# Kernel tuning notes

Measured on AMD Instinct MI355X. Metric: run time of the kernel, lower is better.

## Reference

```python
import jax, jax.numpy as jnp
import numpy as np

N, D, H, L, T, R = 50000, 128, 8, 2, 4, 8
E = 800000
HD = D // H  # head_size = 16
SQRT_D = float(np.sqrt(HD))


def typed_linear(x, types, W):
    # x: (n, Din), types: (n,), W: (T, Din, Dout)  -- per-type dense projection
    out = jnp.zeros((x.shape[0], W.shape[-1]), x.dtype)
    for t in range(W.shape[0]):
        out = out + jnp.where((types == t)[:, None], x @ W[t], 0.0)
    return out


def rel_typed(x, etype, W):
    # x: (E, H, d), etype: (E,), W: (H, R, d, d) -- per-head, per-edge-type linear
    out = jnp.zeros_like(x)
    for r in range(W.shape[1]):
        out = out + jnp.where((etype == r)[:, None, None], jnp.einsum('ehd,hdo->eho', x, W[:, r]), 0.0)
    return out


def edge_softmax(a, dst, n):
    # softmax over incoming edges per destination node, per head. a: (E, H)
    amax = jax.ops.segment_max(a, dst, num_segments=n)
    amax = jnp.where(jnp.isfinite(amax), amax, 0.0)
    ex = jnp.exp(a - amax[dst])
    s = jax.ops.segment_sum(ex, dst, num_segments=n)
    return ex / (s[dst] + 1e-9)


def layer_norm(x, g, b, eps=1e-5):
    mu = x.mean(-1, keepdims=True)
    var = ((x - mu) ** 2).mean(-1, keepdims=True)
    return (x - mu) * jax.lax.rsqrt(var + eps) * g + b


def hgt_conv(x, ntype, etype, src, dst, Wk, Wq, Wv, Wa, ratt, rmsg, rpri, skip):
    n = x.shape[0]
    k = typed_linear(x, ntype, Wk).reshape(n, H, HD)
    q = typed_linear(x, ntype, Wq).reshape(n, H, HD)
    v = typed_linear(x, ntype, Wv).reshape(n, H, HD)
    kw = rel_typed(k[src], etype, ratt)               # (E, H, d)
    pri = rpri[:, etype].T                            # (E, H)
    a = (kw * q[dst]).sum(-1) * pri / SQRT_D          # (E, H)
    m = rel_typed(v[src], etype, rmsg)                # (E, H, d)
    att = edge_softmax(a, dst, n)                     # (E, H)
    h = jax.ops.segment_sum(m * att[..., None], dst, num_segments=n)
    h = h.reshape(n, D)
    h = typed_linear(h, ntype, Wa)                    # dropout off (eval)
    alpha = jax.nn.sigmoid(skip[ntype])[:, None]
    return h * alpha + x * (1.0 - alpha)


def setup_inputs() -> dict:
    key = jax.random.key(0)
    ks = jax.random.split(key, 12)
    g_lin = float(np.sqrt(2.0 / (D + D)))   # xavier-ish scale for D x D
    g_rel = float(np.sqrt(2.0 / (HD + HD)))
    g_emb = float(np.sqrt(2.0 / (N + D)))
    return {
        'embed': jax.random.normal(ks[0], (T, N, D), jnp.float32) * g_emb,
        'Wk': jax.random.normal(ks[1], (L, T, D, D), jnp.float32) * g_lin,
        'Wq': jax.random.normal(ks[2], (L, T, D, D), jnp.float32) * g_lin,
        'Wv': jax.random.normal(ks[3], (L, T, D, D), jnp.float32) * g_lin,
        'Wa': jax.random.normal(ks[4], (L, T, D, D), jnp.float32) * g_lin,
        'rel_att': jax.random.normal(ks[5], (L, H, R, HD, HD), jnp.float32) * g_rel,
        'rel_msg': jax.random.normal(ks[6], (L, H, R, HD, HD), jnp.float32) * g_rel,
        'rel_pri': jnp.ones((L, H, R), jnp.float32),
        'skip': jnp.ones((L, T), jnp.float32),
        'ln_g': jnp.ones((L, D), jnp.float32),
        'ln_b': jnp.zeros((L, D), jnp.float32),
        'src': jax.random.randint(ks[7], (E,), 0, N, jnp.int32),
        'dst': jax.random.randint(ks[8], (E,), 0, N, jnp.int32),
        'ntype': jax.random.randint(ks[9], (N,), 0, T, jnp.int32),
        'etype': jax.random.randint(ks[10], (E,), 0, R, jnp.int32),
    }


def reference(embed, Wk, Wq, Wv, Wa, rel_att, rel_msg, rel_pri, skip, ln_g, ln_b, src, dst, ntype, etype):
    # masked per-type embedding init: node gets row <rank-within-its-type> of its type table
    onehot = jax.nn.one_hot(ntype, T, dtype=jnp.int32)
    rank = jnp.take_along_axis(jnp.cumsum(onehot, axis=0), ntype[:, None], axis=1)[:, 0] - 1
    h = embed[ntype, rank]                            # (N, D)
    for l in range(L):
        h_prev = h
        hc = hgt_conv(h, ntype, etype, src, dst,
                      Wk[l], Wq[l], Wv[l], Wa[l],
                      rel_att[l], rel_msg[l], rel_pri[l], skip[l])
        h = layer_norm(hc, ln_g[l], ln_b[l]) + h_prev
    return h
```

## Files before the change

### kernel.cpp

```cpp
#include <hip/hip_runtime.h>
#include <math.h>

#define N_NODES 50000
#define DIM     128
#define NHEAD   8
#define HDIM    16
#define NLAYER  2
#define NTYPE   4
#define NREL    8
#define NEDGE   800000
#define RB      256
#define GN      8
#define MT      32
#define NK      (N_NODES * NREL)

typedef __attribute__((ext_vector_type(8))) short bf16x8;
typedef __attribute__((ext_vector_type(4))) float f32x4;

__device__ __forceinline__ float blo(unsigned w) { return __uint_as_float(w << 16); }
__device__ __forceinline__ float bhi(unsigned w) { return __uint_as_float(w & 0xFFFF0000u); }
__device__ __forceinline__ unsigned short f2bf(float f) {
    unsigned b = __float_as_uint(f);
    b += 0x7FFFu + ((b >> 16) & 1u);
    return (unsigned short)(b >> 16);
}
__device__ __forceinline__ bf16x8 pack8(float4 x0, float4 x1) {
    bf16x8 r;
    r[0] = (short)f2bf(x0.x); r[1] = (short)f2bf(x0.y);
    r[2] = (short)f2bf(x0.z); r[3] = (short)f2bf(x0.w);
    r[4] = (short)f2bf(x1.x); r[5] = (short)f2bf(x1.y);
    r[6] = (short)f2bf(x1.z); r[7] = (short)f2bf(x1.w);
    return r;
}


__global__ void k_hist(const int* __restrict__ ntype, int* __restrict__ hist, int n) {
    __shared__ int cnt[NTYPE];
    if (threadIdx.x < NTYPE) cnt[threadIdx.x] = 0;
    __syncthreads();
    int i = blockIdx.x * RB + threadIdx.x;
    if (i < n) atomicAdd(&cnt[ntype[i]], 1);
    __syncthreads();
    if (threadIdx.x < NTYPE) hist[blockIdx.x * NTYPE + threadIdx.x] = cnt[threadIdx.x];
}

__global__ void k_prefix(const int* __restrict__ hist, int* __restrict__ off, int nb) {
    int t = threadIdx.x;
    if (t >= NTYPE) return;
    int acc = 0;
    for (int b = 0; b < nb; b++) { off[b * NTYPE + t] = acc; acc += hist[b * NTYPE + t]; }
}

__global__ void k_rank(const int* __restrict__ ntype, const int* __restrict__ off,
                       int* __restrict__ rank, int n) {
    __shared__ int ty[RB];
    int i = blockIdx.x * RB + threadIdx.x;
    int t = (i < n) ? ntype[i] : -1;
    ty[threadIdx.x] = t;
    __syncthreads();
    if (i < n) {
        int c = 0;
        for (int j = 0; j < (int)threadIdx.x; j++) c += (ty[j] == t);
        rank[i] = off[blockIdx.x * NTYPE + t] + c;
    }
}

__global__ void k_embed(const float* __restrict__ embed, const int* __restrict__ ntype,
                        const int* __restrict__ rank, float* __restrict__ h) {
    int i = blockIdx.x;
    int t = ntype[i], r = rank[i];
    h[(size_t)i * DIM + threadIdx.x] = embed[((size_t)t * N_NODES + r) * DIM + threadIdx.x];
}

__global__ void k_typeoff(const int* __restrict__ hist, const int* __restrict__ boff,
                          int nb, int* __restrict__ typeoff) {
    if (threadIdx.x == 0 && blockIdx.x == 0) {
        int acc = 0;
        for (int t = 0; t < NTYPE; t++) {
            typeoff[t] = acc;
            acc += boff[(nb - 1) * NTYPE + t] + hist[(nb - 1) * NTYPE + t];
        }
    }
}

__global__ void k_perm(const int* __restrict__ ntype, const int* __restrict__ rank,
                       const int* __restrict__ typeoff, int* __restrict__ perm,
                       int* __restrict__ iperm, int n) {
    int i = blockIdx.x * 256 + threadIdx.x;
    if (i < n) {
        int p = typeoff[ntype[i]] + rank[i];
        perm[p] = i;
        iperm[i] = p;
    }
}


__global__ void k_deg2(const int* __restrict__ dst, const int* __restrict__ etype,
                       int* __restrict__ deg) {
    int e = blockIdx.x * 256 + threadIdx.x;
    if (e < NEDGE) atomicAdd(&deg[dst[e] * NREL + etype[e]], 1);
}

__global__ void k_scan1(const int* __restrict__ deg, int* __restrict__ rs,
                        int* __restrict__ bsum, int n) {
    __shared__ int sh[256];
    int i = blockIdx.x * 256 + threadIdx.x;
    int v = (i < n) ? deg[i] : 0;
    sh[threadIdx.x] = v;
    __syncthreads();
    for (int off = 1; off < 256; off <<= 1) {
        int x = (threadIdx.x >= off) ? sh[threadIdx.x - off] : 0;
        __syncthreads();
        sh[threadIdx.x] += x;
        __syncthreads();
    }
    if (i < n) rs[i] = sh[threadIdx.x] - v;
    if (threadIdx.x == 255) bsum[blockIdx.x] = sh[255];
}

__global__ void k_scan2b(int* __restrict__ bsum, int nb) {
    __shared__ int sh[256];
    __shared__ int carry;
    if (threadIdx.x == 0) carry = 0;
    __syncthreads();
    for (int base = 0; base < nb; base += 256) {
        int i = base + threadIdx.x;
        int v = (i < nb) ? bsum[i] : 0;
        sh[threadIdx.x] = v;
        __syncthreads();
        for (int off = 1; off < 256; off <<= 1) {
            int x = (threadIdx.x >= off) ? sh[threadIdx.x - off] : 0;
            __syncthreads();
            sh[threadIdx.x] += x;
            __syncthreads();
        }
        if (i < nb) bsum[i] = sh[threadIdx.x] - v + carry;
        __syncthreads();
        if (threadIdx.x == 0) carry += sh[255];
        __syncthreads();
    }
}

__global__ void k_scan3(int* __restrict__ rs, const int* __restrict__ bsum, int n) {
    int i = blockIdx.x * 256 + threadIdx.x;
    if (i < n) rs[i] += bsum[blockIdx.x];
    if (i == 0) rs[n] = NEDGE;
}

__global__ void k_scatter2(const int* __restrict__ src, const int* __restrict__ dst,
                           const int* __restrict__ etype, const int* __restrict__ iperm,
                           const int* __restrict__ rs,
                           int* __restrict__ cur, int* __restrict__ epk) {
    int e = blockIdx.x * 256 + threadIdx.x;
    if (e < NEDGE) {
        int et = etype[e];
        int key = dst[e] * NREL + et;
        int p = atomicAdd(&cur[key], 1);
        epk[rs[key] + p] = iperm[src[e]] | (et << 24);
    }
}


__global__ void k_rattB(const float* __restrict__ ratt, unsigned short* __restrict__ rattB) {
    int i = blockIdx.x * 256 + threadIdx.x;
    rattB[i] = f2bf(ratt[i]);
}

__global__ void k_rmsgT(const float* __restrict__ rmsg, float* __restrict__ rmsgT) {
    int b = blockIdx.x;
    int d = threadIdx.x >> 4, o = threadIdx.x & 15;
    rmsgT[b * 256 + o * 16 + d] = rmsg[b * 256 + d * 16 + o];
}

__global__ void k_packW_all(const float* __restrict__ Wk, const float* __restrict__ Wq,
                            const float* __restrict__ Wv, unsigned short* __restrict__ wpk) {
    int bid = blockIdx.x;
    int t = bid & 3;
    int m = (bid >> 2) % 3;
    int l = bid / 12;
    const float* W = (m == 0 ? Wk : (m == 1 ? Wq : Wv)) + ((size_t)l * NTYPE + t) * 16384;
    unsigned short* ob = wpk + (size_t)bid * 16384;
    for (int idx = threadIdx.x; idx < 16384; idx += 256) {
        int ct = idx >> 11, kc = (idx >> 9) & 3, ln = (idx >> 3) & 63, j = idx & 7;
        int k = kc * 32 + ((ln >> 4) << 3) + j;
        int c = ct * 16 + (ln & 15);
        ob[idx] = f2bf(W[k * 128 + c]);
    }
}


__global__ __launch_bounds__(256) void k_qkv_mfma(
        const float* __restrict__ h, const int* __restrict__ perm, const int* __restrict__ ntype,
        const float* __restrict__ Wk, const float* __restrict__ Wq, const float* __restrict__ Wv,
        const unsigned short* __restrict__ WkB, const unsigned short* __restrict__ WqB,
        const unsigned short* __restrict__ WvB, const float* __restrict__ rmsgT,
        unsigned short* __restrict__ kb, float* __restrict__ qout,
        unsigned short* __restrict__ vt, int n) {
    int tid = threadIdx.x;
    int base = blockIdx.x * MT;
    __shared__ int nodes_s[MT];
    __shared__ int types_s[MT];
    __shared__ float vs[MT][132];

    if (tid < MT) {
        int idx = base + tid;
        int nd = (idx < n) ? perm[idx] : -1;
        nodes_s[tid] = nd;
        types_s[tid] = (nd >= 0) ? ntype[nd] : -1;
    }
    __syncthreads();
    bool same = (nodes_s[MT - 1] >= 0) && (types_s[0] == types_s[MT - 1]);
    int l = tid & 63, w = tid >> 6;

    if (same) {
        int t = types_s[0];
        const unsigned short* wbk = WkB + (size_t)t * 16384;
        const unsigned short* wbq = WqB + (size_t)t * 16384;
        const unsigned short* wbv = WvB + (size_t)t * 16384;
        f32x4 acc[3][2][2];
        #pragma unroll
        for (int m = 0; m < 3; m++)
            #pragma unroll
            for (int a = 0; a < 2; a++)
                #pragma unroll
                for (int b = 0; b < 2; b++) {
                    acc[m][a][b][0] = 0.f; acc[m][a][b][1] = 0.f;
                    acc[m][a][b][2] = 0.f; acc[m][a][b][3] = 0.f;
                }
        #pragma unroll 1
        for (int kc = 0; kc < 4; kc++) {
            int koff = kc * 32 + ((l >> 4) << 3);
            int r0 = l & 15;
            const float4* p0 = (const float4*)(h + (size_t)nodes_s[r0] * DIM + koff);
            bf16x8 a0 = pack8(p0[0], p0[1]);
            const float4* p1 = (const float4*)(h + (size_t)nodes_s[16 + r0] * DIM + koff);
            bf16x8 a1 = pack8(p1[0], p1[1]);
            #pragma unroll
            for (int cti = 0; cti < 2; cti++) {
                int boff = ((w * 2 + cti) * 4 + kc) * 512 + l * 8;
                bf16x8 bk = *(const bf16x8*)(wbk + boff);
                acc[0][0][cti] = __builtin_amdgcn_mfma_f32_16x16x32_bf16(a0, bk, acc[0][0][cti], 0, 0, 0);
                acc[0][1][cti] = __builtin_amdgcn_mfma_f32_16x16x32_bf16(a1, bk, acc[0][1][cti], 0, 0, 0);
                bf16x8 bq = *(const bf16x8*)(wbq + boff);
                acc[1][0][cti] = __builtin_amdgcn_mfma_f32_16x16x32_bf16(a0, bq, acc[1][0][cti], 0, 0, 0);
                acc[1][1][cti] = __builtin_amdgcn_mfma_f32_16x16x32_bf16(a1, bq, acc[1][1][cti], 0, 0, 0);
                bf16x8 bv = *(const bf16x8*)(wbv + boff);
                acc[2][0][cti] = __builtin_amdgcn_mfma_f32_16x16x32_bf16(a0, bv, acc[2][0][cti], 0, 0, 0);
                acc[2][1][cti] = __builtin_amdgcn_mfma_f32_16x16x32_bf16(a1, bv, acc[2][1][cti], 0, 0, 0);
            }
        }
        #pragma unroll
        for (int mt = 0; mt < 2; mt++)
            #pragma unroll
            for (int cti = 0; cti < 2; cti++) {
                int col = w * 32 + cti * 16 + (l & 15);
                #pragma unroll
                for (int r = 0; r < 4; r++) {
                    int row = mt * 16 + ((l >> 4) << 2) + r;
                    size_t p = (size_t)(base + row) * DIM + col;
                    kb[p] = f2bf(acc[0][mt][cti][r]);
                    qout[p] = acc[1][mt][cti][r];
                    vs[row][col] = acc[2][mt][cti][r];
                }
            }
    } else {
        int o = tid & 127, half = tid >> 7;
        for (int nn = half; nn < MT; nn += 2) {
            int nd = nodes_s[nn];
            if (nd < 0) { vs[nn][o] = 0.f; continue; }
            int t = types_s[nn];
            const float* wk = Wk + (size_t)t * 16384;
            const float* wq = Wq + (size_t)t * 16384;
            const float* wv = Wv + (size_t)t * 16384;
            float ak = 0.f, aq = 0.f, av = 0.f;
            for (int d = 0; d < DIM; d++) {
                float xv = h[(size_t)nd * DIM + d];
                ak = fmaf(xv, wk[d * DIM + o], ak);
                aq = fmaf(xv, wq[d * DIM + o], aq);
                av = fmaf(xv, wv[d * DIM + o], av);
            }
            size_t p = (size_t)(base + nn) * DIM + o;
            kb[p] = f2bf(ak); qout[p] = aq;
            vs[nn][o] = av;
        }
    }
    __syncthreads();
    {
        int o = tid & 127, half = tid >> 7;
        int hh = o >> 4, oo = o & 15;
        #pragma unroll 1
        for (int et = 0; et < NREL; et++) {
            const float4* w4 = (const float4*)(rmsgT + ((size_t)(hh * NREL + et) * HDIM + oo) * HDIM);
            float4 w0 = w4[0], w1 = w4[1], w2 = w4[2], w3 = w4[3];
            for (int i = 0; i < 16; i++) {
                int nn = half * 16 + i;
                if (base + nn >= n) continue;
                const float4* v4 = (const float4*)&vs[nn][hh * HDIM];
                float4 v0 = v4[0], v1 = v4[1], v2 = v4[2], v3 = v4[3];
                float a2 = v0.x*w0.x + v0.y*w0.y + v0.z*w0.z + v0.w*w0.w
                         + v1.x*w1.x + v1.y*w1.y + v1.z*w1.z + v1.w*w1.w
                         + v2.x*w2.x + v2.y*w2.y + v2.z*w2.z + v2.w*w2.w
                         + v3.x*w3.x + v3.y*w3.y + v3.z*w3.z + v3.w*w3.w;
                vt[((size_t)(base + nn) * NREL + et) * DIM + o] = f2bf(a2);
            }
        }
    }
}


__global__ __launch_bounds__(128) void k_fused11(
        const unsigned short* __restrict__ kb, const float* __restrict__ qbuf,
        const unsigned short* __restrict__ vt,
        const int* __restrict__ perm,
        const int* __restrict__ rs2, const int* __restrict__ epk,
        const unsigned short* __restrict__ rattB, const float* __restrict__ rpri,
        float* __restrict__ agg) {
    int b = blockIdx.x;
    int node = perm[b];
    int tid = threadIdx.x;
    int hh = tid >> 4, oo = tid & 15;
    int wv = tid >> 6;
    int hl = hh & 3;

    __shared__ float q_s[DIM];
    __shared__ float u_s[NREL][NHEAD * HDIM + 4];
    __shared__ float a_sw[2][4][HDIM + 1];
    __shared__ int   es_sw[2][HDIM];

    int e0 = rs2[node * NREL];
    int e1 = rs2[node * NREL + NREL];
    if (e0 == e1) { agg[(size_t)b * DIM + tid] = 0.f; return; }

    q_s[tid] = qbuf[(size_t)b * DIM + tid];
    {
        const float4* q4 = (const float4*)&q_s[hh * HDIM];
        float4 q0 = q4[0], q1 = q4[1], q2 = q4[2], q3 = q4[3];
        #pragma unroll
        for (int et = 0; et < NREL; et++) {
            const uint4* wB = (const uint4*)(rattB + ((size_t)(hh * NREL + et) * HDIM + oo) * HDIM);
            uint4 wa = wB[0], wb = wB[1];
            float s = blo(wa.x)*q0.x + bhi(wa.x)*q0.y + blo(wa.y)*q0.z + bhi(wa.y)*q0.w
                    + blo(wa.z)*q1.x + bhi(wa.z)*q1.y + blo(wa.w)*q1.z + bhi(wa.w)*q1.w
                    + blo(wb.x)*q2.x + bhi(wb.x)*q2.y + blo(wb.y)*q2.z + bhi(wb.y)*q2.w
                    + blo(wb.z)*q3.x + bhi(wb.z)*q3.y + blo(wb.w)*q3.z + bhi(wb.w)*q3.w;
            u_s[et][tid] = s * rpri[hh * NREL + et] * 0.25f;
        }
    }

    float m_h = -1e30f, s_h = 0.f, out = 0.f;

    for (int w0e = e0; w0e < e1; w0e += HDIM) {
        int cnt = min(HDIM, e1 - w0e);
        float a = -1e30f;
        int pk = 0;
        if (oo < cnt) {
            pk = epk[w0e + oo];
            int sv = pk & 0x00FFFFFF;
            int et = ((unsigned)pk) >> 24;
            const uint4* kr = (const uint4*)(kb + (size_t)sv * DIM + hh * HDIM);
            uint4 ka = kr[0], kc = kr[1];
            const float4* u4 = (const float4*)&u_s[et][hh * HDIM];
            float4 u0 = u4[0], u1 = u4[1], u2 = u4[2], u3 = u4[3];
            a = blo(ka.x)*u0.x + bhi(ka.x)*u0.y + blo(ka.y)*u0.z + bhi(ka.y)*u0.w
              + blo(ka.z)*u1.x + bhi(ka.z)*u1.y + blo(ka.w)*u1.z + bhi(ka.w)*u1.w
              + blo(kc.x)*u2.x + bhi(kc.x)*u2.y + blo(kc.y)*u2.z + bhi(kc.y)*u2.w
              + blo(kc.z)*u3.x + bhi(kc.z)*u3.y + blo(kc.w)*u3.z + bhi(kc.w)*u3.w;
        }
        if (hl == 0) es_sw[wv][oo] = pk;
        float cmax = a;
        cmax = fmaxf(cmax, __shfl_xor(cmax, 1));
        cmax = fmaxf(cmax, __shfl_xor(cmax, 2));
        cmax = fmaxf(cmax, __shfl_xor(cmax, 4));
        cmax = fmaxf(cmax, __shfl_xor(cmax, 8));
        float m_t = (cmax > m_h + 12.f) ? cmax : m_h;
        float r = __expf(m_h - m_t);
        s_h *= r; out *= r; m_h = m_t;
        float p = (oo < cnt) ? __expf(a - m_h) : 0.f;
        float ps = p;
        ps += __shfl_xor(ps, 1);
        ps += __shfl_xor(ps, 2);
        ps += __shfl_xor(ps, 4);
        ps += __shfl_xor(ps, 8);
        s_h += ps;
        a_sw[wv][hl][oo] = p;
        for (int c = 0; c < cnt; c++) {
            float pc = a_sw[wv][hl][c];
            int pkc = es_sw[wv][c];
            int sv = pkc & 0x00FFFFFF;
            int et = ((unsigned)pkc) >> 24;
            unsigned short uv = vt[((size_t)sv * NREL + et) * DIM + tid];
            out = fmaf(pc, __uint_as_float((unsigned)uv << 16), out);
        }
    }

    agg[(size_t)b * DIM + tid] = out / (s_h + 1e-9f);
}


__global__ __launch_bounds__(128) void k_out_g(
        const float* __restrict__ agg, float* __restrict__ h,
        const int* __restrict__ perm, const int* __restrict__ ntype,
        const float* __restrict__ Wa, const float* __restrict__ skip,
        const float* __restrict__ ln_g, const float* __restrict__ ln_b, int n) {
    int o = threadIdx.x;
    int base = blockIdx.x * GN;
    __shared__ float xs[GN][DIM];
    __shared__ float hcs[GN][DIM + 1];
    __shared__ int nodes[GN];
    __shared__ int types[GN];
    __shared__ float mu_s[GN], rs_s[GN];
    if (o < GN) {
        int idx = base + o;
        int nd = (idx < n) ? perm[idx] : -1;
        nodes[o] = nd;
        types[o] = (nd >= 0) ? ntype[nd] : -1;
    }
    __syncthreads();
    #pragma unroll
    for (int nn = 0; nn < GN; nn++)
        if (nodes[nn] >= 0) xs[nn][o] = agg[(size_t)(base + nn) * DIM + o];
    __syncthreads();
    bool same = (nodes[GN - 1] >= 0) && (types[0] == types[GN - 1]);
    if (same) {
        int t = types[0];
        const float* w = Wa + (size_t)t * DIM * DIM;
        float acc[GN];
        #pragma unroll
        for (int nn = 0; nn < GN; nn++) acc[nn] = 0.f;
        for (int d = 0; d < DIM; d++) {
            float wv = w[d * DIM + o];
            #pragma unroll
            for (int nn = 0; nn < GN; nn++) acc[nn] = fmaf(xs[nn][d], wv, acc[nn]);
        }
        float alpha = 1.f / (1.f + __expf(-skip[t]));
        #pragma unroll
        for (int nn = 0; nn < GN; nn++) {
            float hp = h[(size_t)nodes[nn] * DIM + o];
            hcs[nn][o] = acc[nn] * alpha + hp * (1.f - alpha);
        }
    } else {
        #pragma unroll 1
        for (int nn = 0; nn < GN; nn++) {
            if (nodes[nn] < 0) continue;
            int t = types[nn];
            const float* w = Wa + (size_t)t * DIM * DIM;
            float a0 = 0.f;
            for (int d = 0; d < DIM; d++) a0 = fmaf(xs[nn][d], w[d * DIM + o], a0);
            float alpha = 1.f / (1.f + __expf(-skip[t]));
            float hp = h[(size_t)nodes[nn] * DIM + o];
            hcs[nn][o] = a0 * alpha + hp * (1.f - alpha);
        }
    }
    __syncthreads();
    {
        int g = o >> 4, j = o & 15;
        if (nodes[g] >= 0) {
            float s = 0.f;
            for (int d = j; d < DIM; d += 16) s += hcs[g][d];
            #pragma unroll
            for (int m = 1; m < 16; m <<= 1) s += __shfl_xor(s, m);
            float mu = s * (1.f / DIM);
            float v = 0.f;
            for (int d = j; d < DIM; d += 16) { float dv = hcs[g][d] - mu; v = fmaf(dv, dv, v); }
            #pragma unroll
            for (int m = 1; m < 16; m <<= 1) v += __shfl_xor(v, m);
            if (j == 0) { mu_s[g] = mu; rs_s[g] = rsqrtf(v * (1.f / DIM) + 1e-5f); }
        }
    }
    __syncthreads();
    float g_o = ln_g[o], b_o = ln_b[o];
    #pragma unroll
    for (int nn = 0; nn < GN; nn++) {
        if (nodes[nn] >= 0) {
            float hp = h[(size_t)nodes[nn] * DIM + o];
            h[(size_t)nodes[nn] * DIM + o] = (hcs[nn][o] - mu_s[nn]) * rs_s[nn] * g_o + b_o + hp;
        }
    }
}


extern "C" void kernel_launch(void* const* d_in, const int* in_sizes, int n_in,
                              void* d_out, int out_size, void* d_ws, size_t ws_size,
                              hipStream_t stream) {
    const float* embed = (const float*)d_in[0];
    const float* Wk    = (const float*)d_in[1];
    const float* Wq    = (const float*)d_in[2];
    const float* Wv    = (const float*)d_in[3];
    const float* Wa    = (const float*)d_in[4];
    const float* ratt  = (const float*)d_in[5];
    const float* rmsg  = (const float*)d_in[6];
    const float* rpri  = (const float*)d_in[7];
    const float* skip  = (const float*)d_in[8];
    const float* ln_g  = (const float*)d_in[9];
    const float* ln_b  = (const float*)d_in[10];
    const int*   src   = (const int*)d_in[11];
    const int*   dst   = (const int*)d_in[12];
    const int*   ntype = (const int*)d_in[13];
    const int*   etype = (const int*)d_in[14];

    float* h = (float*)d_out;

    const size_t ND = (size_t)N_NODES * DIM;
    const int nb = (N_NODES + RB - 1) / RB;
    unsigned short* kb = (unsigned short*)d_ws;
    float* qbuf = (float*)(kb + ND);
    int* rs2  = (int*)(qbuf + ND);
    int* deg2 = rs2 + (NK + 1);
    int* cur2 = deg2 + NK;
    int* epk  = cur2 + NK;
    int* bsum = epk + NEDGE;
    int* rank = bsum + 2048;
    int* hist = rank + N_NODES;
    int* boff = hist + nb * NTYPE;
    int* typeoff = boff + nb * NTYPE;
    int* perm = typeoff + NTYPE;
    int* iperm = perm + N_NODES;
    float* rmsgT = (float*)(iperm + N_NODES);
    unsigned short* rattB = (unsigned short*)(rmsgT + (size_t)NLAYER * NHEAD * NREL * 256);
    unsigned short* vt = rattB + (size_t)NLAYER * NHEAD * NREL * 256;
    unsigned short* wpk = vt + (size_t)N_NODES * NREL * DIM;
    float* agg = qbuf;

    const int EB = (NEDGE + 255) / 256;
    const int nb2 = (NK + 255) / 256;

    k_hist<<<nb, RB, 0, stream>>>(ntype, hist, N_NODES);
    k_prefix<<<1, 64, 0, stream>>>(hist, boff, nb);
    k_rank<<<nb, RB, 0, stream>>>(ntype, boff, rank, N_NODES);
    k_embed<<<N_NODES, DIM, 0, stream>>>(embed, ntype, rank, h);
    k_typeoff<<<1, 64, 0, stream>>>(hist, boff, nb, typeoff);
    k_perm<<<nb, 256, 0, stream>>>(ntype, rank, typeoff, perm, iperm, N_NODES);

    hipMemsetAsync(deg2, 0, (size_t)NK * sizeof(int), stream);
    hipMemsetAsync(cur2, 0, (size_t)NK * sizeof(int), stream);
    k_deg2<<<EB, 256, 0, stream>>>(dst, etype, deg2);
    k_scan1<<<nb2, 256, 0, stream>>>(deg2, rs2, bsum, NK);
    k_scan2b<<<1, 256, 0, stream>>>(bsum, nb2);
    k_scan3<<<nb2, 256, 0, stream>>>(rs2, bsum, NK);
    k_scatter2<<<EB, 256, 0, stream>>>(src, dst, etype, iperm, rs2, cur2, epk);

    k_rattB<<<NLAYER * NHEAD * NREL, 256, 0, stream>>>(ratt, rattB);
    k_rmsgT<<<NLAYER * NHEAD * NREL, 256, 0, stream>>>(rmsg, rmsgT);
    k_packW_all<<<NLAYER * 3 * NTYPE, 256, 0, stream>>>(Wk, Wq, Wv, wpk);

    const int NGB = N_NODES / GN;
    const int NMB = (N_NODES + MT - 1) / MT;

    for (int l = 0; l < NLAYER; l++) {
        const float* Wk_l = Wk + (size_t)l * NTYPE * DIM * DIM;
        const float* Wq_l = Wq + (size_t)l * NTYPE * DIM * DIM;
        const float* Wv_l = Wv + (size_t)l * NTYPE * DIM * DIM;
        const float* Wa_l = Wa + (size_t)l * NTYPE * DIM * DIM;
        const unsigned short* wkB_l = wpk + ((size_t)l * 3 + 0) * NTYPE * 16384;
        const unsigned short* wqB_l = wpk + ((size_t)l * 3 + 1) * NTYPE * 16384;
        const unsigned short* wvB_l = wpk + ((size_t)l * 3 + 2) * NTYPE * 16384;
        const unsigned short* rattB_l = rattB + (size_t)l * NHEAD * NREL * 256;
        const float* rmsgT_l = rmsgT + (size_t)l * NHEAD * NREL * 256;
        const float* rpri_l = rpri + (size_t)l * NHEAD * NREL;
        const float* skip_l = skip + (size_t)l * NTYPE;
        const float* g_l = ln_g + (size_t)l * DIM;
        const float* b_l = ln_b + (size_t)l * DIM;

        k_qkv_mfma<<<NMB, 256, 0, stream>>>(h, perm, ntype, Wk_l, Wq_l, Wv_l,
                                            wkB_l, wqB_l, wvB_l, rmsgT_l,
                                            kb, qbuf, vt, N_NODES);
        k_fused11<<<N_NODES, 128, 0, stream>>>(kb, qbuf, vt, perm, rs2, epk,
                                               rattB_l, rpri_l, agg);
        k_out_g<<<NGB, 128, 0, stream>>>(agg, h, perm, ntype, Wa_l, skip_l, g_l, b_l, N_NODES);
    }
}
```

Measured before the change: 755.6 us.

## Precompute per-relation key and message tables per node with MFMA

Instead of applying the per-head, per-relation att and msg matrices on every edge in the aggregation kernel, the QKV kernel now computes transformed K and V for all 8 relation types per node using MFMA, with priority and 1/sqrt(d) folded into the att weights. A new edge kernel simply gathers the precomputed bf16 rows by (src, etype). This trades per-edge matmul work for a much larger node-side table write and gather bandwidth. The path is only enabled when the workspace is large enough, otherwise the old path is used.

```diff
diff --git a/kernel.cpp b/kernel.cpp
--- a/kernel.cpp
+++ b/kernel.cpp
@@ -13,6 +13,7 @@
 #define GN      8
 #define MT      32
 #define NK      (N_NODES * NREL)
+#define LHR     (NLAYER * NHEAD * NREL)
 
 typedef __attribute__((ext_vector_type(8))) short bf16x8;
 typedef __attribute__((ext_vector_type(4))) float f32x4;
@@ -30,6 +31,12 @@
     r[2] = (short)f2bf(x0.z); r[3] = (short)f2bf(x0.w);
     r[4] = (short)f2bf(x1.x); r[5] = (short)f2bf(x1.y);
     r[6] = (short)f2bf(x1.z); r[7] = (short)f2bf(x1.w);
+    return r;
+}
+__device__ __forceinline__ bf16x8 zero8() {
+    bf16x8 r;
+    #pragma unroll
+    for (int j = 0; j < 8; j++) r[j] = 0;
     return r;
 }
 
@@ -170,6 +177,31 @@
     int b = blockIdx.x;
     int d = threadIdx.x >> 4, o = threadIdx.x & 15;
     rmsgT[b * 256 + o * 16 + d] = rmsg[b * 256 + d * 16 + o];
+}
+
+__global__ void k_rmsgBP(const float* __restrict__ rmsg, unsigned short* __restrict__ out) {
+    int b = blockIdx.x;
+    int i = threadIdx.x;
+    int ln = i >> 3, e = i & 7;
+    int half = ln >> 4;
+    unsigned short v = 0;
+    if (half < 2) v = f2bf(rmsg[(size_t)b * 256 + (half * 8 + e) * 16 + (ln & 15)]);
+    out[(size_t)b * 512 + i] = v;
+}
+
+__global__ void k_rattBP(const float* __restrict__ ratt, const float* __restrict__ rpri,
+                         unsigned short* __restrict__ out) {
+    int b = blockIdx.x;
+    int i = threadIdx.x;
+    int ln = i >> 3, e = i & 7;
+    int half = ln >> 4;
+    int et = b % NREL;
+    int hh = (b / NREL) % NHEAD;
+    int l = b / (NREL * NHEAD);
+    float scale = rpri[(l * NHEAD + hh) * NREL + et] * 0.25f;
+    unsigned short v = 0;
+    if (half < 2) v = f2bf(ratt[(size_t)b * 256 + (half * 8 + e) * 16 + (ln & 15)] * scale);
+    out[(size_t)b * 512 + i] = v;
 }
 
 __global__ void k_packW_all(const float* __restrict__ Wk, const float* __restrict__ Wq,
@@ -189,18 +221,21 @@
 }
 
 
+template<int FULL>
 __global__ __launch_bounds__(256) void k_qkv_mfma(
         const float* __restrict__ h, const int* __restrict__ perm, const int* __restrict__ ntype,
         const float* __restrict__ Wk, const float* __restrict__ Wq, const float* __restrict__ Wv,
         const unsigned short* __restrict__ WkB, const unsigned short* __restrict__ WqB,
         const unsigned short* __restrict__ WvB, const float* __restrict__ rmsgT,
+        const unsigned short* __restrict__ rattBP, const unsigned short* __restrict__ rmsgBP,
         unsigned short* __restrict__ kb, float* __restrict__ qout,
-        unsigned short* __restrict__ vt, int n) {
+        unsigned short* __restrict__ vt, unsigned short* __restrict__ tab, int n) {
     int tid = threadIdx.x;
     int base = blockIdx.x * MT;
     __shared__ int nodes_s[MT];
     __shared__ int types_s[MT];
     __shared__ float vs[MT][132];
+    __shared__ float ks[MT][132];
 
     if (tid < MT) {
         int idx = base + tid;
@@ -258,16 +293,17 @@
                 for (int r = 0; r < 4; r++) {
                     int row = mt * 16 + ((l >> 4) << 2) + r;
                     size_t p = (size_t)(base + row) * DIM + col;
-                    kb[p] = f2bf(acc[0][mt][cti][r]);
                     qout[p] = acc[1][mt][cti][r];
                     vs[row][col] = acc[2][mt][cti][r];
+                    if constexpr (FULL) ks[row][col] = acc[0][mt][cti][r];
+                    else                kb[p] = f2bf(acc[0][mt][cti][r]);
                 }
             }
     } else {
         int o = tid & 127, half = tid >> 7;
         for (int nn = half; nn < MT; nn += 2) {
             int nd = nodes_s[nn];
-            if (nd < 0) { vs[nn][o] = 0.f; continue; }
+            if (nd < 0) { vs[nn][o] = 0.f; if constexpr (FULL) ks[nn][o] = 0.f; continue; }
             int t = types_s[nn];
             const float* wk = Wk + (size_t)t * 16384;
             const float* wq = Wq + (size_t)t * 16384;
@@ -280,12 +316,55 @@
                 av = fmaf(xv, wv[d * DIM + o], av);
             }
             size_t p = (size_t)(base + nn) * DIM + o;
-            kb[p] = f2bf(ak); qout[p] = aq;
+            qout[p] = aq;
             vs[nn][o] = av;
-        }
-    }
-    __syncthreads();
-    {
+            if constexpr (FULL) ks[nn][o] = ak;
+            else                kb[p] = f2bf(ak);
+        }
+    }
+    __syncthreads();
+
+    if constexpr (FULL) {
+        int half = l >> 4;
+        #pragma unroll 1
+        for (int tbl = 0; tbl < 2; tbl++) {
+            const unsigned short* bp = tbl ? rmsgBP : rattBP;
+            bf16x8 afr[2][2];
+            #pragma unroll
+            for (int hh2 = 0; hh2 < 2; hh2++) {
+                int hh = w * 2 + hh2;
+                #pragma unroll
+                for (int nt = 0; nt < 2; nt++) {
+                    if (half < 2) {
+                        const float* srow = tbl ? &vs[nt * 16 + (l & 15)][hh * HDIM + half * 8]
+                                                : &ks[nt * 16 + (l & 15)][hh * HDIM + half * 8];
+                        const float4* vp = (const float4*)srow;
+                        afr[hh2][nt] = pack8(vp[0], vp[1]);
+                    } else afr[hh2][nt] = zero8();
+                }
+            }
+            #pragma unroll 1
+            for (int hh2 = 0; hh2 < 2; hh2++) {
+                int hh = w * 2 + hh2;
+                #pragma unroll 1
+                for (int et = 0; et < NREL; et++) {
+                    bf16x8 bfr = *(const bf16x8*)(bp + ((size_t)(hh * NREL + et) * 64 + l) * 8);
+                    #pragma unroll
+                    for (int nt = 0; nt < 2; nt++) {
+                        f32x4 d4 = {0.f, 0.f, 0.f, 0.f};
+                        d4 = __builtin_amdgcn_mfma_f32_16x16x32_bf16(afr[hh2][nt], bfr, d4, 0, 0, 0);
+                        #pragma unroll
+                        for (int r = 0; r < 4; r++) {
+                            int row = nt * 16 + half * 4 + r;
+                            if (base + row < n)
+                                tab[((size_t)(base + row) * NREL + et) * 256 + tbl * 128
+                                    + hh * HDIM + (l & 15)] = f2bf(d4[r]);
+                        }
+                    }
+                }
+            }
+        }
+    } else {
         int o = tid & 127, half = tid >> 7;
         int hh = o >> 4, oo = o & 15;
         #pragma unroll 1
@@ -305,6 +384,78 @@
             }
         }
     }
+}
+
+
+__global__ __launch_bounds__(128) void k_fused12(
+        const unsigned short* __restrict__ tab, const float* __restrict__ qbuf,
+        const int* __restrict__ perm,
+        const int* __restrict__ rs2, const int* __restrict__ epk,
+        float* __restrict__ agg) {
+    int b = blockIdx.x;
+    int node = perm[b];
+    int tid = threadIdx.x;
+    int hh = tid >> 4, oo = tid & 15;
+    int wv = tid >> 6;
+    int hl = hh & 3;
+
+    __shared__ float q_s[DIM];
+    __shared__ float a_sw[2][4][HDIM + 1];
+    __shared__ int   es_sw[2][HDIM];
+
+    int e0 = rs2[node * NREL];
+    int e1 = rs2[node * NREL + NREL];
+    if (e0 == e1) { agg[(size_t)b * DIM + tid] = 0.f; return; }
+
+    q_s[tid] = qbuf[(size_t)b * DIM + tid];
+    const float4* q4 = (const float4*)&q_s[hh * HDIM];
+    float4 q0 = q4[0], q1 = q4[1], q2 = q4[2], q3 = q4[3];
+
+    float m_h = -1e30f, s_h = 0.f, out = 0.f;
+
+    for (int w0e = e0; w0e < e1; w0e += HDIM) {
+        int cnt = min(HDIM, e1 - w0e);
+        float a = -1e30f;
+        int pk = 0;
+        if (oo < cnt) {
+            pk = epk[w0e + oo];
+            int sv = pk & 0x00FFFFFF;
+            int et = ((unsigned)pk) >> 24;
+            const uint4* kw = (const uint4*)(tab + ((size_t)sv * NREL + et) * 256 + hh * HDIM);
+            uint4 ka = kw[0], kc = kw[1];
+            a = blo(ka.x)*q0.x + bhi(ka.x)*q0.y + blo(ka.y)*q0.z + bhi(ka.y)*q0.w
+              + blo(ka.z)*q1.x + bhi(ka.z)*q1.y + blo(ka.w)*q1.z + bhi(ka.w)*q1.w
+              + blo(kc.x)*q2.x + bhi(kc.x)*q2.y + blo(kc.y)*q2.z + bhi(kc.y)*q2.w
+              + blo(kc.z)*q3.x + bhi(kc.z)*q3.y + blo(kc.w)*q3.z + bhi(kc.w)*q3.w;
+        }
+        if (hl == 0) es_sw[wv][oo] = pk;
+        float cmax = a;
+        cmax = fmaxf(cmax, __shfl_xor(cmax, 1));
+        cmax = fmaxf(cmax, __shfl_xor(cmax, 2));
+        cmax = fmaxf(cmax, __shfl_xor(cmax, 4));
+        cmax = fmaxf(cmax, __shfl_xor(cmax, 8));
+        float m_t = (cmax > m_h + 12.f) ? cmax : m_h;
+        float r = __expf(m_h - m_t);
+        s_h *= r; out *= r; m_h = m_t;
+        float p = (oo < cnt) ? __expf(a - m_h) : 0.f;
+        float ps = p;
+        ps += __shfl_xor(ps, 1);
+        ps += __shfl_xor(ps, 2);
+        ps += __shfl_xor(ps, 4);
+        ps += __shfl_xor(ps, 8);
+        s_h += ps;
+        a_sw[wv][hl][oo] = p;
+        for (int c = 0; c < cnt; c++) {
+            float pc = a_sw[wv][hl][c];
+            int pkc = es_sw[wv][c];
+            int sv = pkc & 0x00FFFFFF;
+            int et = ((unsigned)pkc) >> 24;
+            unsigned short uv = tab[((size_t)sv * NREL + et) * 256 + 128 + tid];
+            out = fmaf(pc, __uint_as_float((unsigned)uv << 16), out);
+        }
+    }
+
+    agg[(size_t)b * DIM + tid] = out / (s_h + 1e-9f);
 }
 
 
@@ -516,9 +667,14 @@
     int* perm = typeoff + NTYPE;
     int* iperm = perm + N_NODES;
     float* rmsgT = (float*)(iperm + N_NODES);
-    unsigned short* rattB = (unsigned short*)(rmsgT + (size_t)NLAYER * NHEAD * NREL * 256);
-    unsigned short* vt = rattB + (size_t)NLAYER * NHEAD * NREL * 256;
-    unsigned short* wpk = vt + (size_t)N_NODES * NREL * DIM;
+    unsigned short* rattB  = (unsigned short*)(rmsgT + (size_t)LHR * 256);
+    unsigned short* rattBP = rattB + (size_t)LHR * 256;
+    unsigned short* rmsgBP = rattBP + (size_t)LHR * 512;
+    unsigned short* wpk = rmsgBP + (size_t)LHR * 512;
+    unsigned short* vt  = wpk + (size_t)NLAYER * 3 * NTYPE * 16384;
+    unsigned short* tab = vt;
+    size_t need_full = (size_t)((char*)(tab + (size_t)N_NODES * NREL * 256) - (char*)d_ws);
+    const bool FULL = (ws_size >= need_full);
     float* agg = qbuf;
 
     const int EB = (NEDGE + 255) / 256;
@@ -539,8 +695,10 @@
     k_scan3<<<nb2, 256, 0, stream>>>(rs2, bsum, NK);
     k_scatter2<<<EB, 256, 0, stream>>>(src, dst, etype, iperm, rs2, cur2, epk);
 
-    k_rattB<<<NLAYER * NHEAD * NREL, 256, 0, stream>>>(ratt, rattB);
-    k_rmsgT<<<NLAYER * NHEAD * NREL, 256, 0, stream>>>(rmsg, rmsgT);
+    k_rattB<<<LHR, 256, 0, stream>>>(ratt, rattB);
+    k_rmsgT<<<LHR, 256, 0, stream>>>(rmsg, rmsgT);
+    k_rattBP<<<LHR, 512, 0, stream>>>(ratt, rpri, rattBP);
+    k_rmsgBP<<<LHR, 512, 0, stream>>>(rmsg, rmsgBP);
     k_packW_all<<<NLAYER * 3 * NTYPE, 256, 0, stream>>>(Wk, Wq, Wv, wpk);
 
     const int NGB = N_NODES / GN;
@@ -554,18 +712,29 @@
         const unsigned short* wkB_l = wpk + ((size_t)l * 3 + 0) * NTYPE * 16384;
         const unsigned short* wqB_l = wpk + ((size_t)l * 3 + 1) * NTYPE * 16384;
         const unsigned short* wvB_l = wpk + ((size_t)l * 3 + 2) * NTYPE * 16384;
-        const unsigned short* rattB_l = rattB + (size_t)l * NHEAD * NREL * 256;
+        const unsigned short* rattB_l  = rattB + (size_t)l * NHEAD * NREL * 256;
+        const unsigned short* rattBP_l = rattBP + (size_t)l * NHEAD * NREL * 512;
+        const unsigned short* rmsgBP_l = rmsgBP + (size_t)l * NHEAD * NREL * 512;
         const float* rmsgT_l = rmsgT + (size_t)l * NHEAD * NREL * 256;
         const float* rpri_l = rpri + (size_t)l * NHEAD * NREL;
         const float* skip_l = skip + (size_t)l * NTYPE;
         const float* g_l = ln_g + (size_t)l * DIM;
         const float* b_l = ln_b + (size_t)l * DIM;
 
-        k_qkv_mfma<<<NMB, 256, 0, stream>>>(h, perm, ntype, Wk_l, Wq_l, Wv_l,
-                                            wkB_l, wqB_l, wvB_l, rmsgT_l,
-                                            kb, qbuf, vt, N_NODES);
-        k_fused11<<<N_NODES, 128, 0, stream>>>(kb, qbuf, vt, perm, rs2, epk,
-                                               rattB_l, rpri_l, agg);
+        if (FULL) {
+            k_qkv_mfma<1><<<NMB, 256, 0, stream>>>(h, perm, ntype, Wk_l, Wq_l, Wv_l,
+                                                   wkB_l, wqB_l, wvB_l, rmsgT_l,
+                                                   rattBP_l, rmsgBP_l,
+                                                   kb, qbuf, vt, tab, N_NODES);
+            k_fused12<<<N_NODES, 128, 0, stream>>>(tab, qbuf, perm, rs2, epk, agg);
+        } else {
+            k_qkv_mfma<0><<<NMB, 256, 0, stream>>>(h, perm, ntype, Wk_l, Wq_l, Wv_l,
+                                                   wkB_l, wqB_l, wvB_l, rmsgT_l,
+                                                   rattBP_l, rmsgBP_l,
+                                                   kb, qbuf, vt, tab, N_NODES);
+            k_fused11<<<N_NODES, 128, 0, stream>>>(kb, qbuf, vt, perm, rs2, epk,
+                                                   rattB_l, rpri_l, agg);
+        }
         k_out_g<<<NGB, 128, 0, stream>>>(agg, h, perm, ntype, Wa_l, skip_l, g_l, b_l, N_NODES);
     }
 }
```

Result: slower. 869.0 us (+15.0%).
